# Optimization experiments

Measured on AMD Instinct MI355X. Metric: run time of the kernel, lower is better.

## Reference

```python
import jax, jax.numpy as jnp
import numpy as np

B, T, DIM, H, KV, HD = 1, 2048, 2048, 16, 4, 128


def _rope_tables(T, hd):
    half = hd // 2
    inv_freq = 1.0 / (10000.0 ** (np.arange(0, half, dtype=np.float32) / half))
    t = np.arange(T, dtype=np.float32)
    freqs = np.outer(t, inv_freq)                # [T, hd/2]
    emb = np.concatenate([freqs, freqs], axis=-1)  # [T, hd]
    return jnp.asarray(np.cos(emb)), jnp.asarray(np.sin(emb))


def setup_inputs() -> dict:
    key = jax.random.key(0)
    kx, kq, kk, kv, ko = jax.random.split(key, 5)
    s = 0.02
    x = jax.random.normal(kx, (B, T, DIM), dtype=jnp.float32)
    wq = jax.random.normal(kq, (H * HD, DIM), dtype=jnp.float32) * s
    wk = jax.random.normal(kk, (KV * HD, DIM), dtype=jnp.float32) * s
    wv = jax.random.normal(kv, (KV * HD, DIM), dtype=jnp.float32) * s
    wo = jax.random.normal(ko, (DIM, H * HD), dtype=jnp.float32) * s
    cos, sin = _rope_tables(T, HD)
    return {"x": x, "wq": wq, "wk": wk, "wv": wv, "wo": wo, "cos": cos, "sin": sin}


def _rotate_half(u):
    u1, u2 = jnp.split(u, 2, axis=-1)
    return jnp.concatenate([-u2, u1], axis=-1)


def _apply_rope(u, cos, sin):
    # u: [B, T, h, hd]; cos/sin: [T, hd]
    c = cos[None, :, None, :]
    s = sin[None, :, None, :]
    return u * c + _rotate_half(u) * s


def reference(x, wq, wk, wv, wo, cos, sin):
    b, t, dim = x.shape
    hd = cos.shape[1]
    h = wq.shape[0] // hd
    kvh = wk.shape[0] // hd
    rep = h // kvh
    scale = hd ** -0.5

    q = (x @ wq.T).reshape(b, t, h, hd)
    k = (x @ wk.T).reshape(b, t, kvh, hd)
    v = (x @ wv.T).reshape(b, t, kvh, hd)

    q = _apply_rope(q, cos, sin)
    k = _apply_rope(k, cos, sin)

    # Group queries by shared KV head instead of materializing repeat_kv
    qg = q.reshape(b, t, kvh, rep, hd)
    scores = jnp.einsum('bqgrd,bkgd->bgrqk', qg, k) * scale  # [b,g,r,T,T]
    causal = jnp.tril(jnp.ones((t, t), dtype=bool))
    scores = jnp.where(causal[None, None, None], scores, jnp.float32(-1e30))
    attn = jax.nn.softmax(scores, axis=-1)
    out = jnp.einsum('bgrqk,bkgd->bqgrd', attn, v).reshape(b, t, h * hd)
    return out @ wo.T
```

## Files before the change

### kernel.cpp

```cpp
#include <hip/hip_runtime.h>
#include <hip/hip_bf16.h>

typedef unsigned short u16;
typedef __attribute__((ext_vector_type(8))) short bf16x8;
typedef __attribute__((ext_vector_type(4))) float f32x4;

#define T_SEQ 2048
#define DIM   2048
#define NH    16
#define NKV   4
#define HD    128
#define NQKV  3072
#define SCALE 0.08838834764831845f
#define CHUNK 512

__device__ __forceinline__ u16 f2bf(float f) {
  unsigned int u = __float_as_uint(f);
  unsigned int r = (u + 0x7fffu + ((u >> 16) & 1u)) >> 16;
  return (u16)r;
}
__device__ __forceinline__ float bf2f(u16 v) {
  return __uint_as_float(((unsigned int)v) << 16);
}

#define B1 1048576
#define B2 2097152
#define B3 2359296
#define B4 2621440
#define B5 3670016
__global__ void cast_all(const float4* __restrict__ x,  const float4* __restrict__ wq,
                         const float4* __restrict__ wk, const float4* __restrict__ wv,
                         const float4* __restrict__ wo,
                         ushort4* __restrict__ xb, ushort4* __restrict__ wqkvb,
                         ushort4* __restrict__ wob) {
  int i = blockIdx.x * 256 + threadIdx.x;
  const float4* src; ushort4* dst; int j;
  if (i < B1)      { src = x;  dst = xb;               j = i; }
  else if (i < B2) { src = wq; dst = wqkvb;            j = i - B1; }
  else if (i < B3) { src = wk; dst = wqkvb + 1048576;  j = i - B2; }
  else if (i < B4) { src = wv; dst = wqkvb + 1310720;  j = i - B3; }
  else             { src = wo; dst = wob;              j = i - B4; }
  float4 v = src[j];
  ushort4 o;
  o.x = f2bf(v.x); o.y = f2bf(v.y); o.z = f2bf(v.z); o.w = f2bf(v.w);
  dst[j] = o;
}

#define BM 128
#define BN 128
#define BK 64
#define LDP 72

__global__ __launch_bounds__(256) void gemm_bt(
    const u16* __restrict__ A, const u16* __restrict__ W,
    float* __restrict__ Cf, u16* __restrict__ Cb, int M, int N, int K)
{
  __shared__ u16 As[BM * LDP];
  __shared__ u16 Bs[BN * LDP];
  const int tid  = threadIdx.x;
  const int lane = tid & 63;
  const int wave = tid >> 6;
  const int ln   = lane & 15;
  const int quad = lane >> 4;
  const int m0 = blockIdx.y * BM;
  const int n0 = blockIdx.x * BN;
  const int wm = (wave >> 1) * 64;
  const int wn = (wave & 1) * 64;

  const int sr = tid >> 3;
  const int sc = (tid & 7) * 8;

  f32x4 acc[4][4] = {};

  for (int k0 = 0; k0 < K; k0 += BK) {
#pragma unroll
    for (int c = 0; c < 4; ++c) {
      int row = c * 32 + sr;
      *(bf16x8*)&As[row * LDP + sc] =
          *(const bf16x8*)&A[(size_t)(m0 + row) * K + k0 + sc];
      *(bf16x8*)&Bs[row * LDP + sc] =
          *(const bf16x8*)&W[(size_t)(n0 + row) * K + k0 + sc];
    }
    __syncthreads();
#pragma unroll
    for (int ks = 0; ks < 2; ++ks) {
      bf16x8 af[4], bfr[4];
#pragma unroll
      for (int mt = 0; mt < 4; ++mt)
        af[mt] = *(const bf16x8*)&As[(wm + mt * 16 + ln) * LDP + ks * 32 + quad * 8];
#pragma unroll
      for (int nt = 0; nt < 4; ++nt)
        bfr[nt] = *(const bf16x8*)&Bs[(wn + nt * 16 + ln) * LDP + ks * 32 + quad * 8];
#pragma unroll
      for (int mt = 0; mt < 4; ++mt)
#pragma unroll
        for (int nt = 0; nt < 4; ++nt)
          acc[mt][nt] = __builtin_amdgcn_mfma_f32_16x16x32_bf16(
              af[mt], bfr[nt], acc[mt][nt], 0, 0, 0);
    }
    __syncthreads();
  }

#pragma unroll
  for (int mt = 0; mt < 4; ++mt)
#pragma unroll
    for (int nt = 0; nt < 4; ++nt)
#pragma unroll
      for (int r = 0; r < 4; ++r) {
        int row = m0 + wm + mt * 16 + quad * 4 + r;
        int col = n0 + wn + nt * 16 + ln;
        if (Cb) Cb[(size_t)row * N + col] = f2bf(acc[mt][nt][r]);
        else    Cf[(size_t)row * N + col] = acc[mt][nt][r];
      }
}

__global__ void rope_fused(const u16* __restrict__ QKVb,
                           const float* __restrict__ cosT,
                           const float* __restrict__ sinT,
                           u16* __restrict__ Qs, u16* __restrict__ Kb,
                           u16* __restrict__ Vt)
{
  int b = blockIdx.x, d = threadIdx.x;
  if (b < T_SEQ * NH) {
    int t = b >> 4;
    int h = b & 15;
    const u16* row = QKVb + (size_t)t * NQKV + h * HD;
    float u = bf2f(row[d]);
    float pr = (d < 64) ? -bf2f(row[d + 64]) : bf2f(row[d - 64]);
    float c = cosT[t * HD + d], s = sinT[t * HD + d];
    Qs[(size_t)b * HD + d] = f2bf((u * c + pr * s) * SCALE);
  } else if (b < T_SEQ * (NH + NKV)) {
    int b2 = b - T_SEQ * NH;
    int t = b2 >> 2;
    int g = b2 & 3;
    const u16* row = QKVb + (size_t)t * NQKV + DIM + g * HD;
    float u = bf2f(row[d]);
    float pr = (d < 64) ? -bf2f(row[d + 64]) : bf2f(row[d - 64]);
    float c = cosT[t * HD + d], s = sinT[t * HD + d];
    Kb[(size_t)b2 * HD + d] = f2bf(u * c + pr * s);
  } else {
    int b3 = b - T_SEQ * (NH + NKV);
    int idx = b3 * 128 + d;
    int t  = idx & (T_SEQ - 1);
    int dd = (idx >> 11) & (HD - 1);
    int g  = idx >> 18;
    Vt[idx] = QKVb[(size_t)t * NQKV + DIM + NKV * HD + g * HD + dd];
  }
}

#define KSP 136
#define VSP 72
#define PSP 72
__global__ __launch_bounds__(256) void flash_partial(
    const u16* __restrict__ Qs, const u16* __restrict__ Kb,
    const u16* __restrict__ Vt, u16* __restrict__ Opart,
    float* __restrict__ lpart)
{
  const int c  = blockIdx.x;
  const int qi = blockIdx.y;
  const int h  = blockIdx.z;
  const int b  = qi >> 2;
  if (c > b) return;
  const int g  = h >> 2;
  const int q0 = qi << 7;
  const int k0 = c << 9;
  const int kend = min(k0 + CHUNK, q0 + 128);

  __shared__ u16 Ks[64 * KSP];
  __shared__ u16 Vs[HD * VSP];
  __shared__ u16 Ps[4][16 * PSP];

  const int tid  = threadIdx.x;
  const int lane = tid & 63;
  const int w    = tid >> 6;
  const int ln   = lane & 15;
  const int quad = lane >> 4;

  bf16x8 aq[2][4];
#pragma unroll
  for (int mt = 0; mt < 2; ++mt) {
    const u16* qp = Qs + ((size_t)(q0 + w * 32 + mt * 16 + ln) * NH + h) * HD + quad * 8;
#pragma unroll
    for (int ks = 0; ks < 4; ++ks) aq[mt][ks] = *(const bf16x8*)&qp[ks * 32];
  }

  f32x4 o[2][8] = {};
  float rs[2][4] = {};

  for (int jb = k0; jb < kend; jb += 64) {
    {
      int r = tid >> 4, cc = (tid & 15) * 8;
#pragma unroll
      for (int i = 0; i < 4; ++i) {
        int row = i * 16 + r;
        *(bf16x8*)&Ks[row * KSP + cc] =
            *(const bf16x8*)&Kb[((size_t)(jb + row) * NKV + g) * HD + cc];
      }
    }
    {
      int r = tid >> 3, cc = (tid & 7) * 8;
#pragma unroll
      for (int i = 0; i < 4; ++i) {
        int row = i * 32 + r;
        *(bf16x8*)&Vs[row * VSP + cc] =
            *(const bf16x8*)&Vt[(size_t)(g * HD + row) * T_SEQ + jb + cc];
      }
    }
    __syncthreads();

#pragma unroll
    for (int mt = 0; mt < 2; ++mt) {
      const int rbase = q0 + w * 32 + mt * 16 + quad * 4;
      const int rmax  = q0 + w * 32 + mt * 16 + 15;
      if (jb <= rmax) {
        f32x4 sc[4];
#pragma unroll
        for (int nb = 0; nb < 4; ++nb) {
          f32x4 s = {};
#pragma unroll
          for (int ks = 0; ks < 4; ++ks) {
            bf16x8 kf = *(const bf16x8*)&Ks[(nb * 16 + ln) * KSP + ks * 32 + quad * 8];
            s = __builtin_amdgcn_mfma_f32_16x16x32_bf16(aq[mt][ks], kf, s, 0, 0, 0);
          }
          sc[nb] = s;
        }
        const bool diag = (jb >= q0);
#pragma unroll
        for (int nb = 0; nb < 4; ++nb) {
          int j = jb + nb * 16 + ln;
#pragma unroll
          for (int r = 0; r < 4; ++r) {
            float p = (!diag || j <= rbase + r) ? __expf(sc[nb][r]) : 0.f;
            rs[mt][r] += p;
            Ps[w][(quad * 4 + r) * PSP + nb * 16 + ln] = f2bf(p);
          }
        }
#pragma unroll
        for (int kst = 0; kst < 2; ++kst) {
          bf16x8 ap = *(const bf16x8*)&Ps[w][ln * PSP + kst * 32 + quad * 8];
#pragma unroll
          for (int nb8 = 0; nb8 < 8; ++nb8) {
            bf16x8 bv = *(const bf16x8*)&Vs[(nb8 * 16 + ln) * VSP + kst * 32 + quad * 8];
            o[mt][nb8] = __builtin_amdgcn_mfma_f32_16x16x32_bf16(ap, bv, o[mt][nb8], 0, 0, 0);
          }
        }
      }
    }
    __syncthreads();
  }

  const int slot = h * 40 + 2 * b * (b + 1) + (qi & 3) * (b + 1) + c;
  u16*   op = Opart + (size_t)slot * (128 * 128);
  float* lp = lpart + (size_t)slot * 128;
#pragma unroll
  for (int mt = 0; mt < 2; ++mt) {
#pragma unroll
    for (int r = 0; r < 4; ++r)
#pragma unroll
      for (int off = 1; off < 16; off <<= 1)
        rs[mt][r] += __shfl_xor(rs[mt][r], off);
    int rowb = w * 32 + mt * 16 + quad * 4;
#pragma unroll
    for (int r = 0; r < 4; ++r) {
#pragma unroll
      for (int nb8 = 0; nb8 < 8; ++nb8)
        op[(rowb + r) * 128 + nb8 * 16 + ln] = f2bf(o[mt][nb8][r]);
      if (ln == 0) lp[rowb + r] = rs[mt][r];
    }
  }
}

__global__ void flash_reduce(const u16* __restrict__ Opart,
                             const float* __restrict__ lpart,
                             u16* __restrict__ AO)
{
  const int h = blockIdx.y;
  const int d = threadIdx.x & 127;
  const int t = blockIdx.x * 2 + (threadIdx.x >> 7);
  const int qi = t >> 7, r = t & 127;
  const int b = qi >> 2;
  const int base = h * 40 + 2 * b * (b + 1) + (qi & 3) * (b + 1);
  float so = 0.f, sl = 0.f;
  for (int cc = 0; cc <= b; ++cc) {
    so += bf2f(Opart[(size_t)(base + cc) * (128 * 128) + r * 128 + d]);
    sl += lpart[(size_t)(base + cc) * 128 + r];
  }
  AO[(size_t)t * DIM + h * HD + d] = f2bf(so / sl);
}

extern "C" void kernel_launch(void* const* d_in, const int* in_sizes, int n_in,
                              void* d_out, int out_size, void* d_ws, size_t ws_size,
                              hipStream_t stream) {
  const float* x    = (const float*)d_in[0];
  const float* wq   = (const float*)d_in[1];
  const float* wk   = (const float*)d_in[2];
  const float* wv   = (const float*)d_in[3];
  const float* wo   = (const float*)d_in[4];
  const float* cosT = (const float*)d_in[5];
  const float* sinT = (const float*)d_in[6];
  float* out = (float*)d_out;

  char* ws = (char*)d_ws;
  const size_t MB = 1024 * 1024;
  u16*   xb    = (u16*)(ws + 0 * MB);
  u16*   wqkvb = (u16*)(ws + 8 * MB);
  u16*   wob   = (u16*)(ws + 20 * MB);
  u16*   QKVb  = (u16*)(ws + 28 * MB);
  u16*   Qs    = (u16*)(ws + 8 * MB);
  u16*   Kb    = (u16*)(ws + 16 * MB);
  u16*   Vt    = (u16*)(ws + 18 * MB);
  u16*   AO    = (u16*)(ws + 0 * MB);
  u16*   Opart = (u16*)(ws + 28 * MB);
  float* lpart = (float*)(ws + 48 * MB);

  cast_all<<<B5 / 256, 256, 0, stream>>>(
      (const float4*)x, (const float4*)wq, (const float4*)wk, (const float4*)wv,
      (const float4*)wo, (ushort4*)xb, (ushort4*)wqkvb, (ushort4*)wob);

  gemm_bt<<<dim3(NQKV / BN, T_SEQ / BM), 256, 0, stream>>>(
      xb, wqkvb, nullptr, QKVb, T_SEQ, NQKV, DIM);

  rope_fused<<<T_SEQ * (NH + NKV) + (NKV * HD * T_SEQ) / 128, HD, 0, stream>>>(
      QKVb, cosT, sinT, Qs, Kb, Vt);

  flash_partial<<<dim3(4, 16, 16), 256, 0, stream>>>(Qs, Kb, Vt, Opart, lpart);
  flash_reduce<<<dim3(T_SEQ / 2, NH), 256, 0, stream>>>(Opart, lpart, AO);

  gemm_bt<<<dim3(DIM / BN, T_SEQ / BM), 256, 0, stream>>>(
      AO, wob, out, nullptr, T_SEQ, DIM, DIM);
}
```

Measured before the change: 286.1 us.

## Halve flash query tile to 64 rows and use direct global-to-LDS loads in GEMM

The attention kernel now assigns 64 query rows per block (16 per wave) instead of 128, doubling the grid and reworking the partial-slot indexing and reduce kernel to match. The aim is more blocks for better CU occupancy and load balance on the causal triangle, at the cost of loading each K/V tile twice as often. Separately, the GEMM now loads tiles with global_load_lds straight into unpadded LDS, skipping the register round trip. Dropping the padding risks LDS bank conflicts on the MFMA fragment reads.

```diff
diff --git a/kernel.cpp b/kernel.cpp
--- a/kernel.cpp
+++ b/kernel.cpp
@@ -49,14 +49,18 @@
 #define BM 128
 #define BN 128
 #define BK 64
-#define LDP 72
+
+#define GLOAD_LDS16(g, l)                                          \
+  __builtin_amdgcn_global_load_lds(                                \
+      (const __attribute__((address_space(1))) void*)(g),          \
+      (__attribute__((address_space(3))) void*)(l), 16, 0, 0)
 
 __global__ __launch_bounds__(256) void gemm_bt(
     const u16* __restrict__ A, const u16* __restrict__ W,
     float* __restrict__ Cf, u16* __restrict__ Cb, int M, int N, int K)
 {
-  __shared__ u16 As[BM * LDP];
-  __shared__ u16 Bs[BN * LDP];
+  __shared__ u16 As[BM * BK];
+  __shared__ u16 Bs[BN * BK];
   const int tid  = threadIdx.x;
   const int lane = tid & 63;
   const int wave = tid >> 6;
@@ -67,19 +71,17 @@
   const int wm = (wave >> 1) * 64;
   const int wn = (wave & 1) * 64;
 
-  const int sr = tid >> 3;
-  const int sc = (tid & 7) * 8;
+  const int srow = tid >> 3;
+  const int scol = (tid & 7) * 8;
 
   f32x4 acc[4][4] = {};
 
   for (int k0 = 0; k0 < K; k0 += BK) {
 #pragma unroll
-    for (int c = 0; c < 4; ++c) {
-      int row = c * 32 + sr;
-      *(bf16x8*)&As[row * LDP + sc] =
-          *(const bf16x8*)&A[(size_t)(m0 + row) * K + k0 + sc];
-      *(bf16x8*)&Bs[row * LDP + sc] =
-          *(const bf16x8*)&W[(size_t)(n0 + row) * K + k0 + sc];
+    for (int i = 0; i < 4; ++i) {
+      int row = i * 32 + srow;
+      GLOAD_LDS16(&A[(size_t)(m0 + row) * K + k0 + scol], &As[row * BK + scol]);
+      GLOAD_LDS16(&W[(size_t)(n0 + row) * K + k0 + scol], &Bs[row * BK + scol]);
     }
     __syncthreads();
 #pragma unroll
@@ -87,10 +89,10 @@
       bf16x8 af[4], bfr[4];
 #pragma unroll
       for (int mt = 0; mt < 4; ++mt)
-        af[mt] = *(const bf16x8*)&As[(wm + mt * 16 + ln) * LDP + ks * 32 + quad * 8];
+        af[mt] = *(const bf16x8*)&As[(wm + mt * 16 + ln) * BK + ks * 32 + quad * 8];
 #pragma unroll
       for (int nt = 0; nt < 4; ++nt)
-        bfr[nt] = *(const bf16x8*)&Bs[(wn + nt * 16 + ln) * LDP + ks * 32 + quad * 8];
+        bfr[nt] = *(const bf16x8*)&Bs[(wn + nt * 16 + ln) * BK + ks * 32 + quad * 8];
 #pragma unroll
       for (int mt = 0; mt < 4; ++mt)
 #pragma unroll
@@ -159,12 +161,12 @@
   const int c  = blockIdx.x;
   const int qi = blockIdx.y;
   const int h  = blockIdx.z;
-  const int b  = qi >> 2;
+  const int b  = qi >> 3;
   if (c > b) return;
   const int g  = h >> 2;
-  const int q0 = qi << 7;
+  const int q0 = qi << 6;
   const int k0 = c << 9;
-  const int kend = min(k0 + CHUNK, q0 + 128);
+  const int kend = min(k0 + CHUNK, q0 + 64);
 
   __shared__ u16 Ks[64 * KSP];
   __shared__ u16 Vs[HD * VSP];
@@ -176,16 +178,17 @@
   const int ln   = lane & 15;
   const int quad = lane >> 4;
 
-  bf16x8 aq[2][4];
-#pragma unroll
-  for (int mt = 0; mt < 2; ++mt) {
-    const u16* qp = Qs + ((size_t)(q0 + w * 32 + mt * 16 + ln) * NH + h) * HD + quad * 8;
-#pragma unroll
-    for (int ks = 0; ks < 4; ++ks) aq[mt][ks] = *(const bf16x8*)&qp[ks * 32];
-  }
-
-  f32x4 o[2][8] = {};
-  float rs[2][4] = {};
+  bf16x8 aq[4];
+  {
+    const u16* qp = Qs + ((size_t)(q0 + w * 16 + ln) * NH + h) * HD + quad * 8;
+#pragma unroll
+    for (int ks = 0; ks < 4; ++ks) aq[ks] = *(const bf16x8*)&qp[ks * 32];
+  }
+
+  f32x4 o[8] = {};
+  float rs[4] = {};
+
+  const int rbase = q0 + w * 16 + quad * 4;
 
   for (int jb = k0; jb < kend; jb += 64) {
     {
@@ -208,65 +211,57 @@
     }
     __syncthreads();
 
-#pragma unroll
-    for (int mt = 0; mt < 2; ++mt) {
-      const int rbase = q0 + w * 32 + mt * 16 + quad * 4;
-      const int rmax  = q0 + w * 32 + mt * 16 + 15;
-      if (jb <= rmax) {
-        f32x4 sc[4];
-#pragma unroll
-        for (int nb = 0; nb < 4; ++nb) {
-          f32x4 s = {};
-#pragma unroll
-          for (int ks = 0; ks < 4; ++ks) {
-            bf16x8 kf = *(const bf16x8*)&Ks[(nb * 16 + ln) * KSP + ks * 32 + quad * 8];
-            s = __builtin_amdgcn_mfma_f32_16x16x32_bf16(aq[mt][ks], kf, s, 0, 0, 0);
-          }
-          sc[nb] = s;
+    {
+      f32x4 sc[4];
+#pragma unroll
+      for (int nb = 0; nb < 4; ++nb) {
+        f32x4 s = {};
+#pragma unroll
+        for (int ks = 0; ks < 4; ++ks) {
+          bf16x8 kf = *(const bf16x8*)&Ks[(nb * 16 + ln) * KSP + ks * 32 + quad * 8];
+          s = __builtin_amdgcn_mfma_f32_16x16x32_bf16(aq[ks], kf, s, 0, 0, 0);
         }
-        const bool diag = (jb >= q0);
-#pragma unroll
-        for (int nb = 0; nb < 4; ++nb) {
-          int j = jb + nb * 16 + ln;
-#pragma unroll
-          for (int r = 0; r < 4; ++r) {
-            float p = (!diag || j <= rbase + r) ? __expf(sc[nb][r]) : 0.f;
-            rs[mt][r] += p;
-            Ps[w][(quad * 4 + r) * PSP + nb * 16 + ln] = f2bf(p);
-          }
+        sc[nb] = s;
+      }
+      const bool diag = (jb >= q0);
+#pragma unroll
+      for (int nb = 0; nb < 4; ++nb) {
+        int j = jb + nb * 16 + ln;
+#pragma unroll
+        for (int r = 0; r < 4; ++r) {
+          float p = (!diag || j <= rbase + r) ? __expf(sc[nb][r]) : 0.f;
+          rs[r] += p;
+          Ps[w][(quad * 4 + r) * PSP + nb * 16 + ln] = f2bf(p);
         }
-#pragma unroll
-        for (int kst = 0; kst < 2; ++kst) {
-          bf16x8 ap = *(const bf16x8*)&Ps[w][ln * PSP + kst * 32 + quad * 8];
-#pragma unroll
-          for (int nb8 = 0; nb8 < 8; ++nb8) {
-            bf16x8 bv = *(const bf16x8*)&Vs[(nb8 * 16 + ln) * VSP + kst * 32 + quad * 8];
-            o[mt][nb8] = __builtin_amdgcn_mfma_f32_16x16x32_bf16(ap, bv, o[mt][nb8], 0, 0, 0);
-          }
+      }
+#pragma unroll
+      for (int kst = 0; kst < 2; ++kst) {
+        bf16x8 ap = *(const bf16x8*)&Ps[w][ln * PSP + kst * 32 + quad * 8];
+#pragma unroll
+        for (int nb8 = 0; nb8 < 8; ++nb8) {
+          bf16x8 bv = *(const bf16x8*)&Vs[(nb8 * 16 + ln) * VSP + kst * 32 + quad * 8];
+          o[nb8] = __builtin_amdgcn_mfma_f32_16x16x32_bf16(ap, bv, o[nb8], 0, 0, 0);
         }
       }
     }
     __syncthreads();
   }
 
-  const int slot = h * 40 + 2 * b * (b + 1) + (qi & 3) * (b + 1) + c;
-  u16*   op = Opart + (size_t)slot * (128 * 128);
-  float* lp = lpart + (size_t)slot * 128;
-#pragma unroll
-  for (int mt = 0; mt < 2; ++mt) {
-#pragma unroll
-    for (int r = 0; r < 4; ++r)
-#pragma unroll
-      for (int off = 1; off < 16; off <<= 1)
-        rs[mt][r] += __shfl_xor(rs[mt][r], off);
-    int rowb = w * 32 + mt * 16 + quad * 4;
-#pragma unroll
-    for (int r = 0; r < 4; ++r) {
-#pragma unroll
-      for (int nb8 = 0; nb8 < 8; ++nb8)
-        op[(rowb + r) * 128 + nb8 * 16 + ln] = f2bf(o[mt][nb8][r]);
-      if (ln == 0) lp[rowb + r] = rs[mt][r];
-    }
+  const int slot = h * 80 + 4 * b * (b + 1) + (qi & 7) * (b + 1) + c;
+  u16*   op = Opart + (size_t)slot * (64 * 128);
+  float* lp = lpart + (size_t)slot * 64;
+#pragma unroll
+  for (int r = 0; r < 4; ++r)
+#pragma unroll
+    for (int off = 1; off < 16; off <<= 1)
+      rs[r] += __shfl_xor(rs[r], off);
+  const int rowb = w * 16 + quad * 4;
+#pragma unroll
+  for (int r = 0; r < 4; ++r) {
+#pragma unroll
+    for (int nb8 = 0; nb8 < 8; ++nb8)
+      op[(rowb + r) * 128 + nb8 * 16 + ln] = f2bf(o[nb8][r]);
+    if (ln == 0) lp[rowb + r] = rs[r];
   }
 }
 
@@ -277,13 +272,13 @@
   const int h = blockIdx.y;
   const int d = threadIdx.x & 127;
   const int t = blockIdx.x * 2 + (threadIdx.x >> 7);
-  const int qi = t >> 7, r = t & 127;
-  const int b = qi >> 2;
-  const int base = h * 40 + 2 * b * (b + 1) + (qi & 3) * (b + 1);
+  const int qi = t >> 6, r = t & 63;
+  const int b = qi >> 3;
+  const int base = h * 80 + 4 * b * (b + 1) + (qi & 7) * (b + 1);
   float so = 0.f, sl = 0.f;
   for (int cc = 0; cc <= b; ++cc) {
-    so += bf2f(Opart[(size_t)(base + cc) * (128 * 128) + r * 128 + d]);
-    sl += lpart[(size_t)(base + cc) * 128 + r];
+    so += bf2f(Opart[(size_t)(base + cc) * (64 * 128) + r * 128 + d]);
+    sl += lpart[(size_t)(base + cc) * 64 + r];
   }
   AO[(size_t)t * DIM + h * HD + d] = f2bf(so / sl);
 }
@@ -323,7 +318,7 @@
   rope_fused<<<T_SEQ * (NH + NKV) + (NKV * HD * T_SEQ) / 128, HD, 0, stream>>>(
       QKVb, cosT, sinT, Qs, Kb, Vt);
 
-  flash_partial<<<dim3(4, 16, 16), 256, 0, stream>>>(Qs, Kb, Vt, Opart, lpart);
+  flash_partial<<<dim3(4, 32, 16), 256, 0, stream>>>(Qs, Kb, Vt, Opart, lpart);
   flash_reduce<<<dim3(T_SEQ / 2, NH), 256, 0, stream>>>(Opart, lpart, AO);
 
   gemm_bt<<<dim3(DIM / BN, T_SEQ / BM), 256, 0, stream>>>(
```

Result: slower. 325.6 us (+13.8%).

## Double-buffer GEMM with direct global-to-LDS loads; read K/V directly in flash kernel

Applied to the files above, without the earlier changes.

The GEMM now uses global_load_lds to copy A/W tiles straight into two LDS buffers, prefetching the next K-slice while MFMAs run on the current one, and drops the LDS row padding. The flash-attention partial kernel no longer stages K and V in shared memory or syncs between waves. Each wave loads K and V fragments from global memory and processes both 16-row query tiles together, sharing the loaded K and V fragments between them. This removes barriers and LDS copies but loses the padding that avoided bank conflicts and makes each wave fetch K/V independently through cache. The GEMM loop no longer has a visible barrier before the buffer swap (the diff context is truncated), so it may race.

```diff
diff --git a/kernel.cpp b/kernel.cpp
--- a/kernel.cpp
+++ b/kernel.cpp
@@ -49,14 +49,18 @@
 #define BM 128
 #define BN 128
 #define BK 64
-#define LDP 72
+
+#define GLOAD_LDS16(g, l)                                          \
+  __builtin_amdgcn_global_load_lds(                                \
+      (const __attribute__((address_space(1))) void*)(g),          \
+      (__attribute__((address_space(3))) void*)(l), 16, 0, 0)
 
 __global__ __launch_bounds__(256) void gemm_bt(
     const u16* __restrict__ A, const u16* __restrict__ W,
     float* __restrict__ Cf, u16* __restrict__ Cb, int M, int N, int K)
 {
-  __shared__ u16 As[BM * LDP];
-  __shared__ u16 Bs[BN * LDP];
+  __shared__ u16 As[2][BM * BK];
+  __shared__ u16 Bs[2][BN * BK];
   const int tid  = threadIdx.x;
   const int lane = tid & 63;
   const int wave = tid >> 6;
@@ -67,30 +71,42 @@
   const int wm = (wave >> 1) * 64;
   const int wn = (wave & 1) * 64;
 
-  const int sr = tid >> 3;
-  const int sc = (tid & 7) * 8;
+  const int srow = tid >> 3;
+  const int scol = (tid & 7) * 8;
 
   f32x4 acc[4][4] = {};
 
-  for (int k0 = 0; k0 < K; k0 += BK) {
-#pragma unroll
-    for (int c = 0; c < 4; ++c) {
-      int row = c * 32 + sr;
-      *(bf16x8*)&As[row * LDP + sc] =
-          *(const bf16x8*)&A[(size_t)(m0 + row) * K + k0 + sc];
-      *(bf16x8*)&Bs[row * LDP + sc] =
-          *(const bf16x8*)&W[(size_t)(n0 + row) * K + k0 + sc];
-    }
-    __syncthreads();
+#pragma unroll
+  for (int i = 0; i < 4; ++i) {
+    int row = i * 32 + srow;
+    GLOAD_LDS16(&A[(size_t)(m0 + row) * K + scol], &As[0][row * BK + scol]);
+    GLOAD_LDS16(&W[(size_t)(n0 + row) * K + scol], &Bs[0][row * BK + scol]);
+  }
+  __syncthreads();
+
+  const int nk = K / BK;
+  for (int t = 0; t < nk; ++t) {
+    const int cur = t & 1;
+    if (t + 1 < nk) {
+      const int k1 = (t + 1) * BK;
+#pragma unroll
+      for (int i = 0; i < 4; ++i) {
+        int row = i * 32 + srow;
+        GLOAD_LDS16(&A[(size_t)(m0 + row) * K + k1 + scol],
+                    &As[cur ^ 1][row * BK + scol]);
+        GLOAD_LDS16(&W[(size_t)(n0 + row) * K + k1 + scol],
+                    &Bs[cur ^ 1][row * BK + scol]);
+      }
+    }
 #pragma unroll
     for (int ks = 0; ks < 2; ++ks) {
       bf16x8 af[4], bfr[4];
 #pragma unroll
       for (int mt = 0; mt < 4; ++mt)
-        af[mt] = *(const bf16x8*)&As[(wm + mt * 16 + ln) * LDP + ks * 32 + quad * 8];
+        af[mt] = *(const bf16x8*)&As[cur][(wm + mt * 16 + ln) * BK + ks * 32 + quad * 8];
 #pragma unroll
       for (int nt = 0; nt < 4; ++nt)
-        bfr[nt] = *(const bf16x8*)&Bs[(wn + nt * 16 + ln) * LDP + ks * 32 + quad * 8];
+        bfr[nt] = *(const bf16x8*)&Bs[cur][(wn + nt * 16 + ln) * BK + ks * 32 + quad * 8];
 #pragma unroll
       for (int mt = 0; mt < 4; ++mt)
 #pragma unroll
@@ -148,8 +164,6 @@
   }
 }
 
-#define KSP 136
-#define VSP 72
 #define PSP 72
 __global__ __launch_bounds__(256) void flash_partial(
     const u16* __restrict__ Qs, const u16* __restrict__ Kb,
@@ -166,9 +180,7 @@
   const int k0 = c << 9;
   const int kend = min(k0 + CHUNK, q0 + 128);
 
-  __shared__ u16 Ks[64 * KSP];
-  __shared__ u16 Vs[HD * VSP];
-  __shared__ u16 Ps[4][16 * PSP];
+  __shared__ u16 Ps[4][32 * PSP];
 
   const int tid  = threadIdx.x;
   const int lane = tid & 63;
@@ -187,66 +199,56 @@
   f32x4 o[2][8] = {};
   float rs[2][4] = {};
 
+  const int rb0 = q0 + w * 32 + quad * 4;
+  const int rb1 = rb0 + 16;
+  const int rmax1 = q0 + w * 32 + 31;
+
+  const u16* kbase = Kb + (size_t)g * HD;
+  const u16* vbase = Vt + (size_t)g * HD * T_SEQ;
+
   for (int jb = k0; jb < kend; jb += 64) {
-    {
-      int r = tid >> 4, cc = (tid & 15) * 8;
-#pragma unroll
-      for (int i = 0; i < 4; ++i) {
-        int row = i * 16 + r;
-        *(bf16x8*)&Ks[row * KSP + cc] =
-            *(const bf16x8*)&Kb[((size_t)(jb + row) * NKV + g) * HD + cc];
-      }
-    }
-    {
-      int r = tid >> 3, cc = (tid & 7) * 8;
-#pragma unroll
-      for (int i = 0; i < 4; ++i) {
-        int row = i * 32 + r;
-        *(bf16x8*)&Vs[row * VSP + cc] =
-            *(const bf16x8*)&Vt[(size_t)(g * HD + row) * T_SEQ + jb + cc];
-      }
-    }
-    __syncthreads();
-
-#pragma unroll
-    for (int mt = 0; mt < 2; ++mt) {
-      const int rbase = q0 + w * 32 + mt * 16 + quad * 4;
-      const int rmax  = q0 + w * 32 + mt * 16 + 15;
-      if (jb <= rmax) {
-        f32x4 sc[4];
-#pragma unroll
-        for (int nb = 0; nb < 4; ++nb) {
-          f32x4 s = {};
-#pragma unroll
-          for (int ks = 0; ks < 4; ++ks) {
-            bf16x8 kf = *(const bf16x8*)&Ks[(nb * 16 + ln) * KSP + ks * 32 + quad * 8];
-            s = __builtin_amdgcn_mfma_f32_16x16x32_bf16(aq[mt][ks], kf, s, 0, 0, 0);
-          }
-          sc[nb] = s;
+    if (jb > rmax1) continue;
+    const bool do0 = (jb <= rb0 - quad * 4 + 15);
+    const bool diag = (jb >= q0);
+
+#pragma unroll
+    for (int nb = 0; nb < 4; ++nb) {
+      bf16x8 kf[4];
+      const u16* kp = kbase + (size_t)(jb + nb * 16 + ln) * (NKV * HD) + quad * 8;
+#pragma unroll
+      for (int ks = 0; ks < 4; ++ks) kf[ks] = *(const bf16x8*)&kp[ks * 32];
+      f32x4 s0 = {}, s1 = {};
+#pragma unroll
+      for (int ks = 0; ks < 4; ++ks) {
+        if (do0) s0 = __builtin_amdgcn_mfma_f32_16x16x32_bf16(aq[0][ks], kf[ks], s0, 0, 0, 0);
+        s1 = __builtin_amdgcn_mfma_f32_16x16x32_bf16(aq[1][ks], kf[ks], s1, 0, 0, 0);
+      }
+      const int j = jb + nb * 16 + ln;
+#pragma unroll
+      for (int r = 0; r < 4; ++r) {
+        if (do0) {
+          float p = (!diag || j <= rb0 + r) ? __expf(s0[r]) : 0.f;
+          rs[0][r] += p;
+          Ps[w][(quad * 4 + r) * PSP + nb * 16 + ln] = f2bf(p);
         }
-        const bool diag = (jb >= q0);
-#pragma unroll
-        for (int nb = 0; nb < 4; ++nb) {
-          int j = jb + nb * 16 + ln;
-#pragma unroll
-          for (int r = 0; r < 4; ++r) {
-            float p = (!diag || j <= rbase + r) ? __expf(sc[nb][r]) : 0.f;
-            rs[mt][r] += p;
-            Ps[w][(quad * 4 + r) * PSP + nb * 16 + ln] = f2bf(p);
-          }
-        }
-#pragma unroll
-        for (int kst = 0; kst < 2; ++kst) {
-          bf16x8 ap = *(const bf16x8*)&Ps[w][ln * PSP + kst * 32 + quad * 8];
-#pragma unroll
-          for (int nb8 = 0; nb8 < 8; ++nb8) {
-            bf16x8 bv = *(const bf16x8*)&Vs[(nb8 * 16 + ln) * VSP + kst * 32 + quad * 8];
-            o[mt][nb8] = __builtin_amdgcn_mfma_f32_16x16x32_bf16(ap, bv, o[mt][nb8], 0, 0, 0);
-          }
-        }
-      }
-    }
-    __syncthreads();
+        float p1 = (!diag || j <= rb1 + r) ? __expf(s1[r]) : 0.f;
+        rs[1][r] += p1;
+        Ps[w][(16 + quad * 4 + r) * PSP + nb * 16 + ln] = f2bf(p1);
+      }
+    }
+
+#pragma unroll
+    for (int kst = 0; kst < 2; ++kst) {
+      bf16x8 ap0, ap1;
+      if (do0) ap0 = *(const bf16x8*)&Ps[w][ln * PSP + kst * 32 + quad * 8];
+      ap1 = *(const bf16x8*)&Ps[w][(16 + ln) * PSP + kst * 32 + quad * 8];
+#pragma unroll
+      for (int nb8 = 0; nb8 < 8; ++nb8) {
+        bf16x8 bv = *(const bf16x8*)&vbase[(size_t)(nb8 * 16 + ln) * T_SEQ + jb + kst * 32 + quad * 8];
+        if (do0) o[0][nb8] = __builtin_amdgcn_mfma_f32_16x16x32_bf16(ap0, bv, o[0][nb8], 0, 0, 0);
+        o[1][nb8] = __builtin_amdgcn_mfma_f32_16x16x32_bf16(ap1, bv, o[1][nb8], 0, 0, 0);
+      }
+    }
   }
 
   const int slot = h * 40 + 2 * b * (b + 1) + (qi & 3) * (b + 1) + c;
```

Result: slower. 357.0 us (+24.8%).
